# Kernel tuning notes

Measured on AMD Instinct MI355X. Metric: run time of the kernel, lower is better.

The kernel has to match this reference:

```python
import jax, jax.numpy as jnp
import numpy as np

C = 1024
D = C // 8      # query/key channels
R = C // 16     # channel-attention reduction
B, H, W = 4, 64, 64


def setup_inputs() -> dict:
    key = jax.random.key(0)
    ks = jax.random.split(key, 10)
    s = lambda k, shp, fan: jax.random.normal(k, shp, jnp.float32) * (1.0 / np.sqrt(fan))
    return {
        "x": jax.random.normal(ks[0], (B, C, H, W), jnp.float32),
        "x1": jax.random.normal(ks[1], (B, C, H, W), jnp.float32),
        "Wq": s(ks[2], (D, C), C), "bq": jnp.zeros((D,), jnp.float32),
        "Wk": s(ks[3], (D, C), C), "bk": jnp.zeros((D,), jnp.float32),
        "Wv": s(ks[4], (C, C), C), "bv": jnp.zeros((C,), jnp.float32),
        "Wca1": s(ks[5], (R, C), C),  # CBAM MLP, no bias
        "Wca2": s(ks[6], (C, R), R),
    }


def _forward(x, x1, Wq, bq, Wk, bk, Wv, bv, Wca1, Wca2):
    b, c, h, w = x.shape
    n = h * w
    # 1x1 convs as channel matmuls
    Q = (jnp.einsum('bchw,dc->bdhw', x, Wq) + bq[:, None, None]).reshape(b, D, n)   # [B,D,N]
    K = (jnp.einsum('bchw,dc->bdhw', x, Wk) + bk[:, None, None]).reshape(b, D, n)   # [B,D,N]
    V = (jnp.einsum('bchw,oc->bohw', x1, Wv) + bv[:, None, None]).reshape(b, c, n)  # [B,C,N]
    # energy[b,n,m] = Q[:,n] . K[:,m]
    energy = jnp.einsum('bdn,bdm->bnm', Q, K)
    att = jax.nn.sigmoid(energy)                       # [B,N,N]
    # torch: bmm(V, att^T) -> out[b,c,n] = sum_m V[b,c,m] * att[b,n,m]
    out = jnp.einsum('bcm,bnm->bcn', V, att).reshape(b, c, h, w)
    # ChannelAttention (CBAM): shared MLP on avg+max pooled features, sigmoid gate
    avg = out.mean(axis=(2, 3))                        # [B,C]
    mx = out.max(axis=(2, 3))                          # [B,C]
    mlp = lambda v: jnp.einsum('cr,br->bc', Wca2, jax.nn.relu(jnp.einsum('rc,bc->br', Wca1, v)))
    gate = jax.nn.sigmoid(mlp(avg) + mlp(mx))          # [B,C]
    return out * gate[:, :, None, None]


def reference(x, x1, Wq, bq, Wk, bk, Wv, bv, Wca1, Wca2):
    return _forward(x, x1, Wq, bq, Wk, bk, Wv, bv, Wca1, Wca2)
```

## Files before the change

### kernel.cpp

```cpp
#include <hip/hip_runtime.h>
#include <hip/hip_fp16.h>
#include <cstdint>

typedef _Float16 f16;
typedef __attribute__((ext_vector_type(8))) _Float16 half8;
typedef __attribute__((ext_vector_type(4))) float floatx4;

#define CC 1024
#define DD 128
#define RRR 64
#define BBATCH 4
#define NNN 4096

#define BM 128
#define BN 128

__device__ __forceinline__ void gl_lds16(const void* g, void* l) {
  __builtin_amdgcn_global_load_lds(
      (__attribute__((address_space(1))) void*)(uintptr_t)g,
      (__attribute__((address_space(3))) void*)l, 16, 0, 0);
}

template<int EPI, int BKT>
__global__ __launch_bounds__(256)
void gemm_bt(const f16* __restrict__ A, const f16* __restrict__ Bp, void* __restrict__ Cout,
             const float* __restrict__ bias, int M, int N, int K,
             int lda, int ldb, int ldc, size_t sA, size_t sB, size_t sC)
{
  constexpr int GPR = BKT / 8;
  constexpr int LOG2GPR = (BKT == 64) ? 3 : 4;
  constexpr int GIT = (BM * GPR) / 256;
  __shared__ __align__(16) f16 S[2 * BM * BKT];
  f16* As = S;
  f16* Bs = S + BM * BKT;

  const int z = blockIdx.z;
  const int tid  = threadIdx.x;
  const int lane = tid & 63;
  const int wave = tid >> 6;
  const int m0 = blockIdx.y * BM;
  const int n0 = blockIdx.x * BN;
  const int wm = (wave >> 1) * 64;
  const int wn = (wave & 1) * 64;
  const int quad = lane >> 4;
  const int r16  = lane & 15;
  const int rs   = r16 & 7;

  const f16* Ab = A  + (size_t)z * sA + (size_t)m0 * lda;
  const f16* Bb = Bp + (size_t)z * sB + (size_t)n0 * ldb;

  floatx4 acc[4][4];
#pragma unroll
  for (int i = 0; i < 4; ++i)
#pragma unroll
    for (int j = 0; j < 4; ++j)
      acc[i][j] = (floatx4){0.f, 0.f, 0.f, 0.f};

  int srow[GIT], ssrc[GIT];
#pragma unroll
  for (int r = 0; r < GIT; ++r) {
    const int gi = r * 256 + tid;
    const int row = gi >> LOG2GPR;
    const int gc  = gi & (GPR - 1);
    srow[r] = row;
    ssrc[r] = ((gc ^ (row & 7)) << 3);
  }

  for (int k0 = 0; k0 < K; k0 += BKT) {
#pragma unroll
    for (int r = 0; r < GIT; ++r) {
      gl_lds16(Ab + (size_t)srow[r] * lda + k0 + ssrc[r], As + (size_t)(r * 256 + tid) * 8);
      gl_lds16(Bb + (size_t)srow[r] * ldb + k0 + ssrc[r], Bs + (size_t)(r * 256 + tid) * 8);
    }
    __syncthreads();

#pragma unroll
    for (int kk = 0; kk < BKT; kk += 32) {
      const int kg = kk >> 3;
      half8 af[4], bfr[4];
#pragma unroll
      for (int i = 0; i < 4; ++i)
        af[i] = *(const half8*)(As + (wm + i * 16 + r16) * BKT + (((quad + kg) ^ rs) << 3));
#pragma unroll
      for (int j = 0; j < 4; ++j)
        bfr[j] = *(const half8*)(Bs + (wn + j * 16 + r16) * BKT + (((quad + kg) ^ rs) << 3));
#pragma unroll
      for (int i = 0; i < 4; ++i)
#pragma unroll
        for (int j = 0; j < 4; ++j)
          acc[i][j] = __builtin_amdgcn_mfma_f32_16x16x32_f16(af[i], bfr[j], acc[i][j], 0, 0, 0);
    }
    __syncthreads();
  }

  if constexpr (EPI == 0) {
    float* Cf = (float*)Cout + (size_t)z * sC;
#pragma unroll
    for (int i = 0; i < 4; ++i)
#pragma unroll
      for (int r = 0; r < 4; ++r) {
        const int row = m0 + wm + i * 16 + quad * 4 + r;
#pragma unroll
        for (int j = 0; j < 4; ++j)
          Cf[(size_t)row * ldc + n0 + wn + j * 16 + r16] = acc[i][j][r];
      }
  } else {
    f16* Ch = (f16*)Cout + (size_t)z * sC;
    f16* Ct = S;
#pragma unroll
    for (int i = 0; i < 4; ++i)
#pragma unroll
      for (int r = 0; r < 4; ++r) {
        const int rl = wm + i * 16 + quad * 4 + r;
#pragma unroll
        for (int j = 0; j < 4; ++j) {
          const int cl = wn + j * 16 + r16;
          const float v = acc[i][j][r];
          f16 h;
          if constexpr (EPI == 1)      h = (f16)(v + bias[m0 + rl]);
          else if constexpr (EPI == 2) h = (f16)(v + bias[n0 + cl]);
          else                         h = (f16)(1.0f / (1.0f + __expf(-v)));
          Ct[rl * BN + ((((cl >> 3) ^ (rl & 7)) << 3) | (cl & 7))] = h;
        }
      }
    __syncthreads();
#pragma unroll
    for (int p = 0; p < 8; ++p) {
      const int idx = p * 256 + tid;
      const int rl = idx >> 4;
      const int g  = idx & 15;
      half8 vv = *(const half8*)(Ct + rl * BN + (((g ^ (rl & 7))) << 3));
      *(half8*)(Ch + (size_t)(m0 + rl) * ldc + n0 + g * 8) = vv;
    }
  }
}

__global__ __launch_bounds__(256)
void prep(const float* __restrict__ Wq, const float* __restrict__ Wk, const float* __restrict__ Wv,
          const float* __restrict__ bq, const float* __restrict__ bk,
          f16* __restrict__ WQKb, f16* __restrict__ Wvb, float* __restrict__ bqk)
{
  const int NV = CC * CC;
  const int NQ = DD * CC;
  int i = blockIdx.x * 256 + threadIdx.x;
  if (i < NV)                    Wvb[i] = (f16)Wv[i];
  else if (i < NV + NQ)          WQKb[i - NV] = (f16)Wq[i - NV];
  else if (i < NV + 2 * NQ)      WQKb[i - NV] = (f16)Wk[i - NV - NQ];
  else if (i < NV + 2 * NQ + 2 * DD) {
    int t = i - NV - 2 * NQ;
    bqk[t] = (t < DD) ? bq[t] : bk[t - DD];
  }
}

__global__ __launch_bounds__(256)
void transpose_cvt(const float* __restrict__ x, const float* __restrict__ x1,
                   f16* __restrict__ ox, f16* __restrict__ ox1, int nb)
{
  const int zz = blockIdx.z;
  const int b  = (zz < nb) ? zz : zz - nb;
  const float* in = ((zz < nb) ? x : x1) + (size_t)b * CC * NNN;
  f16* out = ((zz < nb) ? ox : ox1) + (size_t)b * CC * NNN;
  __shared__ float tile[32][33];
  const int c0 = blockIdx.y * 32;
  const int n0 = blockIdx.x * 32;
  const int tx = threadIdx.x & 31;
  const int ty = threadIdx.x >> 5;
#pragma unroll
  for (int r = 0; r < 32; r += 8)
    tile[ty + r][tx] = in[(size_t)(c0 + ty + r) * NNN + n0 + tx];
  __syncthreads();
#pragma unroll
  for (int r = 0; r < 32; r += 8)
    out[(size_t)(n0 + ty + r) * CC + c0 + tx] = (f16)tile[tx][ty + r];
}

__global__ __launch_bounds__(256)
void rowreduce(const float* __restrict__ X, float* __restrict__ avg, float* __restrict__ mx, int ncols)
{
  const size_t ridx = (size_t)blockIdx.y * gridDim.x + blockIdx.x;
  const float4* p = (const float4*)(X + ridx * ncols);
  float s = 0.f, m = -3.402823466e38f;
  for (int i = threadIdx.x; i < ncols / 4; i += 256) {
    float4 v = p[i];
    s += v.x + v.y + v.z + v.w;
    m = fmaxf(m, fmaxf(fmaxf(v.x, v.y), fmaxf(v.z, v.w)));
  }
#pragma unroll
  for (int o = 32; o > 0; o >>= 1) {
    s += __shfl_down(s, o);
    m = fmaxf(m, __shfl_down(m, o));
  }
  __shared__ float ss[4], sm[4];
  if ((threadIdx.x & 63) == 0) { ss[threadIdx.x >> 6] = s; sm[threadIdx.x >> 6] = m; }
  __syncthreads();
  if (threadIdx.x == 0) {
    s = ss[0] + ss[1] + ss[2] + ss[3];
    m = fmaxf(fmaxf(sm[0], sm[1]), fmaxf(sm[2], sm[3]));
    avg[ridx] = s / (float)ncols;
    mx[ridx] = m;
  }
}

__global__ __launch_bounds__(256)
void mlp_gate(const float* __restrict__ avg, const float* __restrict__ mxv,
              const float* __restrict__ W1, const float* __restrict__ W2,
              float* __restrict__ gate)
{
  const int z = blockIdx.x;
  avg += (size_t)z * CC; mxv += (size_t)z * CC; gate += (size_t)z * CC;
  const int t = threadIdx.x;
  const int r = t & 63;
  const int part = t >> 6;
  __shared__ float pa[4][64], pm[4][64], h[RRR];
  {
    const float* w = W1 + (size_t)r * CC + part * 256;
    const float* av = avg + part * 256;
    const float* mv = mxv + part * 256;
    float sa = 0.f, sm = 0.f;
    for (int c = 0; c < 256; ++c) { float wv = w[c]; sa += wv * av[c]; sm += wv * mv[c]; }
    pa[part][r] = sa; pm[part][r] = sm;
  }
  __syncthreads();
  if (t < RRR) {
    float A_ = pa[0][t] + pa[1][t] + pa[2][t] + pa[3][t];
    float M_ = pm[0][t] + pm[1][t] + pm[2][t] + pm[3][t];
    h[t] = fmaxf(A_, 0.f) + fmaxf(M_, 0.f);
  }
  __syncthreads();
  for (int c = t; c < CC; c += 256) {
    float s = 0.f;
    for (int rr = 0; rr < RRR; ++rr) s += W2[(size_t)c * RRR + rr] * h[rr];
    gate[c] = 1.0f / (1.0f + __expf(-s));
  }
}

__global__ __launch_bounds__(256)
void scale_out(float* __restrict__ out, const float* __restrict__ gate)
{
  out  += (size_t)blockIdx.y * CC * NNN;
  gate += (size_t)blockIdx.y * CC;
  size_t i = (size_t)blockIdx.x * 256 + threadIdx.x;
  float4* p = (float4*)out;
  const float g = gate[(i * 4) >> 12];
  float4 v = p[i];
  v.x *= g; v.y *= g; v.z *= g; v.w *= g;
  p[i] = v;
}

extern "C" void kernel_launch(void* const* d_in, const int* in_sizes, int n_in,
                              void* d_out, int out_size, void* d_ws, size_t ws_size,
                              hipStream_t stream)
{
  const float* x    = (const float*)d_in[0];
  const float* x1   = (const float*)d_in[1];
  const float* Wq   = (const float*)d_in[2];
  const float* bq   = (const float*)d_in[3];
  const float* Wk   = (const float*)d_in[4];
  const float* bk   = (const float*)d_in[5];
  const float* Wv   = (const float*)d_in[6];
  const float* bv   = (const float*)d_in[7];
  const float* Wca1 = (const float*)d_in[8];
  const float* Wca2 = (const float*)d_in[9];
  float* out = (float*)d_out;

  char* ws = (char*)d_ws;
  size_t off = 0;
  auto alloc = [&](size_t bytes) { void* p = ws + off; off += (bytes + 255) & ~255ULL; return p; };

  f16* WQKb = (f16*)alloc((size_t)2 * DD * CC * 2);
  f16* Wvb  = (f16*)alloc((size_t)CC * CC * 2);
  float* bqk  = (float*)alloc(256 * 4);
  float* avg  = (float*)alloc((size_t)BBATCH * CC * 4);
  float* mxv  = (float*)alloc((size_t)BBATCH * CC * 4);
  float* gate = (float*)alloc((size_t)BBATCH * CC * 4);

  const size_t attB = (size_t)NNN * NNN * 2;
  const size_t xTB  = (size_t)BBATCH * NNN * CC * 2;
  const size_t qkB  = (size_t)BBATCH * NNN * 2 * DD * 2;
  const size_t vBB  = (size_t)BBATCH * CC * NNN * 2;
  const size_t fixedEnd = off;

  int g = 0;
  for (int cand = BBATCH; cand >= 1; cand >>= 1) {
    size_t need = fixedEnd + 2 * xTB + qkB + vBB + (size_t)cand * attB + (1 << 20);
    if (need <= ws_size) { g = cand; break; }
  }

  const dim3 blk(256);
  const int prepN = CC * CC + 2 * DD * CC + 2 * DD;
  prep<<<(prepN + 255) / 256, blk, 0, stream>>>(Wq, Wk, Wv, bq, bk, WQKb, Wvb, bqk);

  if (g > 0) {
    f16* xTb  = (f16*)alloc(xTB);
    f16* x1Tb = (f16*)alloc(xTB);
    f16* QKt  = (f16*)alloc(qkB);
    f16* Vb   = (f16*)alloc(vBB);
    f16* att  = (f16*)alloc((size_t)g * attB);

    transpose_cvt<<<dim3(NNN / 32, CC / 32, 2 * BBATCH), blk, 0, stream>>>(x, x1, xTb, x1Tb, BBATCH);

    gemm_bt<2, 64><<<dim3(2 * DD / BN, NNN / BM, BBATCH), blk, 0, stream>>>(
        xTb, WQKb, QKt, bqk, NNN, 2 * DD, CC,
        CC, CC, 2 * DD, (size_t)NNN * CC, 0, (size_t)NNN * 2 * DD);
    gemm_bt<1, 64><<<dim3(NNN / BN, CC / BM, BBATCH), blk, 0, stream>>>(
        Wvb, x1Tb, Vb, bv, CC, NNN, CC,
        CC, CC, NNN, 0, (size_t)NNN * CC, (size_t)CC * NNN);

    for (int b0 = 0; b0 < BBATCH; b0 += g) {
      const int gc = (b0 + g <= BBATCH) ? g : (BBATCH - b0);
      const size_t sQK = (size_t)NNN * 2 * DD;
      gemm_bt<3, 128><<<dim3(NNN / BN, NNN / BM, gc), blk, 0, stream>>>(
          QKt + (size_t)b0 * sQK, QKt + (size_t)b0 * sQK + DD, att, nullptr,
          NNN, NNN, DD, 2 * DD, 2 * DD, NNN, sQK, sQK, (size_t)NNN * NNN);
      gemm_bt<0, 64><<<dim3(NNN / BN, CC / BM, gc), blk, 0, stream>>>(
          Vb + (size_t)b0 * CC * NNN, att, out + (size_t)b0 * CC * NNN, nullptr,
          CC, NNN, NNN, NNN, NNN, NNN,
          (size_t)CC * NNN, (size_t)NNN * NNN, (size_t)CC * NNN);
    }

    rowreduce<<<dim3(CC, BBATCH), blk, 0, stream>>>(out, avg, mxv, NNN);
    mlp_gate<<<BBATCH, blk, 0, stream>>>(avg, mxv, Wca1, Wca2, gate);
    scale_out<<<dim3(CC * NNN / 4 / 256, BBATCH), blk, 0, stream>>>(out, gate);
  } else {
    f16* xTb  = (f16*)alloc((size_t)NNN * CC * 2);
    f16* x1Tb = (f16*)alloc((size_t)NNN * CC * 2);
    f16* QKt  = (f16*)alloc((size_t)NNN * 2 * DD * 2);
    f16* Vb   = (f16*)alloc((size_t)CC * NNN * 2);
    f16* att  = (f16*)alloc(attB);

    for (int b = 0; b < BBATCH; ++b) {
      const float* xb  = x  + (size_t)b * CC * NNN;
      const float* x1b = x1 + (size_t)b * CC * NNN;
      float* outb = out + (size_t)b * CC * NNN;

      transpose_cvt<<<dim3(NNN / 32, CC / 32, 2), blk, 0, stream>>>(xb, x1b, xTb, x1Tb, 1);

      gemm_bt<2, 64><<<dim3(2 * DD / BN, NNN / BM, 1), blk, 0, stream>>>(
          xTb, WQKb, QKt, bqk, NNN, 2 * DD, CC, CC, CC, 2 * DD, 0, 0, 0);
      gemm_bt<1, 64><<<dim3(NNN / BN, CC / BM, 1), blk, 0, stream>>>(
          Wvb, x1Tb, Vb, bv, CC, NNN, CC, CC, CC, NNN, 0, 0, 0);
      gemm_bt<3, 128><<<dim3(NNN / BN, NNN / BM, 1), blk, 0, stream>>>(
          QKt, QKt + DD, att, nullptr, NNN, NNN, DD, 2 * DD, 2 * DD, NNN, 0, 0, 0);
      gemm_bt<0, 64><<<dim3(NNN / BN, CC / BM, 1), blk, 0, stream>>>(
          Vb, att, outb, nullptr, CC, NNN, NNN, NNN, NNN, NNN, 0, 0, 0);

      rowreduce<<<dim3(CC, 1), blk, 0, stream>>>(outb, avg + (size_t)b * CC, mxv + (size_t)b * CC, NNN);
      mlp_gate<<<1, blk, 0, stream>>>(avg + (size_t)b * CC, mxv + (size_t)b * CC, Wca1, Wca2, gate + (size_t)b * CC);
      scale_out<<<dim3(CC * NNN / 4 / 256, 1), blk, 0, stream>>>(outb, gate + (size_t)b * CC);
    }
  }
}
```

Measured before the change: 543.6 us.

## Switch GEMMs to 32x32x16 MFMA and store attention output in fp16

Replaces the 16x16x32 MFMA tiling with 32x32x16 MFMA (2x2 per wave), so each wave issues fewer, larger matrix instructions and does fewer LDS fragment loads. The QK GEMM now uses BK=64 instead of 128. The V·att GEMM writes an fp16 intermediate through the LDS-staged coalesced epilogue instead of scattered fp32 stores. The row-reduce and scale kernels then read fp16 and write the final fp32 output, which cuts intermediate traffic but rounds the pre-gate output to fp16 and needs extra workspace.

```diff
diff --git a/kernel.cpp b/kernel.cpp
--- a/kernel.cpp
+++ b/kernel.cpp
@@ -4,7 +4,7 @@
 
 typedef _Float16 f16;
 typedef __attribute__((ext_vector_type(8))) _Float16 half8;
-typedef __attribute__((ext_vector_type(4))) float floatx4;
+typedef __attribute__((ext_vector_type(16))) float floatx16;
 
 #define CC 1024
 #define DD 128
@@ -14,6 +14,7 @@
 
 #define BM 128
 #define BN 128
+#define BK 64
 
 __device__ __forceinline__ void gl_lds16(const void* g, void* l) {
   __builtin_amdgcn_global_load_lds(
@@ -21,18 +22,15 @@
       (__attribute__((address_space(3))) void*)l, 16, 0, 0);
 }
 
-template<int EPI, int BKT>
-__global__ __launch_bounds__(256)
-void gemm_bt(const f16* __restrict__ A, const f16* __restrict__ Bp, void* __restrict__ Cout,
-             const float* __restrict__ bias, int M, int N, int K,
+template<int EPI>
+__global__ __launch_bounds__(256)
+void gemm_bt(const f16* __restrict__ A, const f16* __restrict__ Bp, f16* __restrict__ Cout,
+             const float* __restrict__ bias, int N, int K,
              int lda, int ldb, int ldc, size_t sA, size_t sB, size_t sC)
 {
-  constexpr int GPR = BKT / 8;
-  constexpr int LOG2GPR = (BKT == 64) ? 3 : 4;
-  constexpr int GIT = (BM * GPR) / 256;
-  __shared__ __align__(16) f16 S[2 * BM * BKT];
+  __shared__ __align__(16) f16 S[2 * BM * BK];
   f16* As = S;
-  f16* Bs = S + BM * BKT;
+  f16* Bs = S + BM * BK;
 
   const int z = blockIdx.z;
   const int tid  = threadIdx.x;
@@ -42,96 +40,85 @@
   const int n0 = blockIdx.x * BN;
   const int wm = (wave >> 1) * 64;
   const int wn = (wave & 1) * 64;
-  const int quad = lane >> 4;
-  const int r16  = lane & 15;
-  const int rs   = r16 & 7;
+  const int l31 = lane & 31;
+  const int hi  = lane >> 5;
+  const int rs  = lane & 7;
 
   const f16* Ab = A  + (size_t)z * sA + (size_t)m0 * lda;
   const f16* Bb = Bp + (size_t)z * sB + (size_t)n0 * ldb;
 
-  floatx4 acc[4][4];
-#pragma unroll
-  for (int i = 0; i < 4; ++i)
-#pragma unroll
-    for (int j = 0; j < 4; ++j)
-      acc[i][j] = (floatx4){0.f, 0.f, 0.f, 0.f};
-
-  int srow[GIT], ssrc[GIT];
-#pragma unroll
-  for (int r = 0; r < GIT; ++r) {
+  floatx16 acc[2][2];
+#pragma unroll
+  for (int i = 0; i < 2; ++i)
+#pragma unroll
+    for (int j = 0; j < 2; ++j)
+#pragma unroll
+      for (int r = 0; r < 16; ++r)
+        acc[i][j][r] = 0.f;
+
+  int srow[4], ssrc[4];
+#pragma unroll
+  for (int r = 0; r < 4; ++r) {
     const int gi = r * 256 + tid;
-    const int row = gi >> LOG2GPR;
-    const int gc  = gi & (GPR - 1);
+    const int row = gi >> 3;
+    const int gc  = gi & 7;
     srow[r] = row;
     ssrc[r] = ((gc ^ (row & 7)) << 3);
   }
 
-  for (int k0 = 0; k0 < K; k0 += BKT) {
-#pragma unroll
-    for (int r = 0; r < GIT; ++r) {
+  for (int k0 = 0; k0 < K; k0 += BK) {
+#pragma unroll
+    for (int r = 0; r < 4; ++r) {
       gl_lds16(Ab + (size_t)srow[r] * lda + k0 + ssrc[r], As + (size_t)(r * 256 + tid) * 8);
       gl_lds16(Bb + (size_t)srow[r] * ldb + k0 + ssrc[r], Bs + (size_t)(r * 256 + tid) * 8);
     }
     __syncthreads();
 
 #pragma unroll
-    for (int kk = 0; kk < BKT; kk += 32) {
-      const int kg = kk >> 3;
-      half8 af[4], bfr[4];
-#pragma unroll
-      for (int i = 0; i < 4; ++i)
-        af[i] = *(const half8*)(As + (wm + i * 16 + r16) * BKT + (((quad + kg) ^ rs) << 3));
-#pragma unroll
-      for (int j = 0; j < 4; ++j)
-        bfr[j] = *(const half8*)(Bs + (wn + j * 16 + r16) * BKT + (((quad + kg) ^ rs) << 3));
-#pragma unroll
-      for (int i = 0; i < 4; ++i)
-#pragma unroll
-        for (int j = 0; j < 4; ++j)
-          acc[i][j] = __builtin_amdgcn_mfma_f32_16x16x32_f16(af[i], bfr[j], acc[i][j], 0, 0, 0);
+    for (int kk = 0; kk < BK; kk += 16) {
+      const int gr = (((kk >> 3) + hi) ^ rs) << 3;
+      half8 af[2], bfr[2];
+#pragma unroll
+      for (int i = 0; i < 2; ++i)
+        af[i] = *(const half8*)(As + (wm + i * 32 + l31) * BK + gr);
+#pragma unroll
+      for (int j = 0; j < 2; ++j)
+        bfr[j] = *(const half8*)(Bs + (wn + j * 32 + l31) * BK + gr);
+#pragma unroll
+      for (int i = 0; i < 2; ++i)
+#pragma unroll
+        for (int j = 0; j < 2; ++j)
+          acc[i][j] = __builtin_amdgcn_mfma_f32_32x32x16_f16(af[i], bfr[j], acc[i][j], 0, 0, 0);
     }
     __syncthreads();
   }
 
-  if constexpr (EPI == 0) {
-    float* Cf = (float*)Cout + (size_t)z * sC;
-#pragma unroll
-    for (int i = 0; i < 4; ++i)
-#pragma unroll
-      for (int r = 0; r < 4; ++r) {
-        const int row = m0 + wm + i * 16 + quad * 4 + r;
-#pragma unroll
-        for (int j = 0; j < 4; ++j)
-          Cf[(size_t)row * ldc + n0 + wn + j * 16 + r16] = acc[i][j][r];
+  f16* Ch = Cout + (size_t)z * sC;
+  f16* Ct = S;
+#pragma unroll
+  for (int i = 0; i < 2; ++i)
+#pragma unroll
+    for (int j = 0; j < 2; ++j)
+#pragma unroll
+      for (int r = 0; r < 16; ++r) {
+        const int rl = wm + i * 32 + (r & 3) + 8 * (r >> 2) + 4 * hi;
+        const int cl = wn + j * 32 + l31;
+        const float v = acc[i][j][r];
+        f16 h;
+        if constexpr (EPI == 0)      h = (f16)v;
+        else if constexpr (EPI == 1) h = (f16)(v + bias[m0 + rl]);
+        else if constexpr (EPI == 2) h = (f16)(v + bias[n0 + cl]);
+        else                         h = (f16)(1.0f / (1.0f + __expf(-v)));
+        Ct[rl * BN + ((((cl >> 3) ^ (rl & 7)) << 3) | (cl & 7))] = h;
       }
-  } else {
-    f16* Ch = (f16*)Cout + (size_t)z * sC;
-    f16* Ct = S;
-#pragma unroll
-    for (int i = 0; i < 4; ++i)
-#pragma unroll
-      for (int r = 0; r < 4; ++r) {
-        const int rl = wm + i * 16 + quad * 4 + r;
-#pragma unroll
-        for (int j = 0; j < 4; ++j) {
-          const int cl = wn + j * 16 + r16;
-          const float v = acc[i][j][r];
-          f16 h;
-          if constexpr (EPI == 1)      h = (f16)(v + bias[m0 + rl]);
-          else if constexpr (EPI == 2) h = (f16)(v + bias[n0 + cl]);
-          else                         h = (f16)(1.0f / (1.0f + __expf(-v)));
-          Ct[rl * BN + ((((cl >> 3) ^ (rl & 7)) << 3) | (cl & 7))] = h;
-        }
-      }
-    __syncthreads();
-#pragma unroll
-    for (int p = 0; p < 8; ++p) {
-      const int idx = p * 256 + tid;
-      const int rl = idx >> 4;
-      const int g  = idx & 15;
-      half8 vv = *(const half8*)(Ct + rl * BN + (((g ^ (rl & 7))) << 3));
-      *(half8*)(Ch + (size_t)(m0 + rl) * ldc + n0 + g * 8) = vv;
-    }
+  __syncthreads();
+#pragma unroll
+  for (int p = 0; p < 8; ++p) {
+    const int idx = p * 256 + tid;
+    const int rl = idx >> 4;
+    const int g  = idx & 15;
+    half8 vv = *(const half8*)(Ct + rl * BN + ((g ^ (rl & 7)) << 3));
+    *(half8*)(Ch + (size_t)(m0 + rl) * ldc + n0 + g * 8) = vv;
   }
 }
 
@@ -175,15 +162,19 @@
 }
 
 __global__ __launch_bounds__(256)
-void rowreduce(const float* __restrict__ X, float* __restrict__ avg, float* __restrict__ mx, int ncols)
+void rowreduce(const f16* __restrict__ X, float* __restrict__ avg, float* __restrict__ mx, int ncols)
 {
   const size_t ridx = (size_t)blockIdx.y * gridDim.x + blockIdx.x;
-  const float4* p = (const float4*)(X + ridx * ncols);
+  const half8* p = (const half8*)(X + ridx * ncols);
   float s = 0.f, m = -3.402823466e38f;
-  for (int i = threadIdx.x; i < ncols / 4; i += 256) {
-    float4 v = p[i];
-    s += v.x + v.y + v.z + v.w;
-    m = fmaxf(m, fmaxf(fmaxf(v.x, v.y), fmaxf(v.z, v.w)));
+  for (int i = threadIdx.x; i < ncols / 8; i += 256) {
+    half8 v = p[i];
+#pragma unroll
+    for (int e = 0; e < 8; ++e) {
+      float f = (float)v[e];
+      s += f;
+      m = fmaxf(m, f);
+    }
   }
 #pragma unroll
   for (int o = 32; o > 0; o >>= 1) {
@@ -235,16 +226,19 @@
 }
 
 __global__ __launch_bounds__(256)
-void scale_out(float* __restrict__ out, const float* __restrict__ gate)
-{
-  out  += (size_t)blockIdx.y * CC * NNN;
+void scale_out(const f16* __restrict__ oh, float* __restrict__ out, const float* __restrict__ gate)
+{
+  oh  += (size_t)blockIdx.y * CC * NNN;
+  out += (size_t)blockIdx.y * CC * NNN;
   gate += (size_t)blockIdx.y * CC;
   size_t i = (size_t)blockIdx.x * 256 + threadIdx.x;
-  float4* p = (float4*)out;
-  const float g = gate[(i * 4) >> 12];
-  float4 v = p[i];
-  v.x *= g; v.y *= g; v.z *= g; v.w *= g;
-  p[i] = v;
+  half8 v = ((const half8*)oh)[i];
+  const float g = gate[(i * 8) >> 12];
+  float4 a = { (float)v[0] * g, (float)v[1] * g, (float)v[2] * g, (float)v[3] * g };
+  float4 b = { (float)v[4] * g, (float)v[5] * g, (float)v[6] * g, (float)v[7] * g };
+  float4* o = (float4*)out;
+  o[2 * i]     = a;
+  o[2 * i + 1] = b;
 }
 
 extern "C" void kernel_launch(void* const* d_in, const int* in_sizes, int n_in,
@@ -278,11 +272,12 @@
   const size_t xTB  = (size_t)BBATCH * NNN * CC * 2;
   const size_t qkB  = (size_t)BBATCH * NNN * 2 * DD * 2;
   const size_t vBB  = (size_t)BBATCH * CC * NNN * 2;
+  const size_t ohB  = (size_t)BBATCH * CC * NNN * 2;
   const size_t fixedEnd = off;
 
   int g = 0;
   for (int cand = BBATCH; cand >= 1; cand >>= 1) {
-    size_t need = fixedEnd + 2 * xTB + qkB + vBB + (size_t)cand * attB + (1 << 20);
+    size_t need = fixedEnd + 2 * xTB + qkB + vBB + ohB + (size_t)cand * attB + (1 << 20);
     if (need <= ws_size) { g = cand; break; }
   }
 
@@ -295,37 +290,39 @@
     f16* x1Tb = (f16*)alloc(xTB);
     f16* QKt  = (f16*)alloc(qkB);
     f16* Vb   = (f16*)alloc(vBB);
+    f16* outh = (f16*)alloc(ohB);
     f16* att  = (f16*)alloc((size_t)g * attB);
 
     transpose_cvt<<<dim3(NNN / 32, CC / 32, 2 * BBATCH), blk, 0, stream>>>(x, x1, xTb, x1Tb, BBATCH);
 
-    gemm_bt<2, 64><<<dim3(2 * DD / BN, NNN / BM, BBATCH), blk, 0, stream>>>(
-        xTb, WQKb, QKt, bqk, NNN, 2 * DD, CC,
+    gemm_bt<2><<<dim3(2 * DD / BN, NNN / BM, BBATCH), blk, 0, stream>>>(
+        xTb, WQKb, QKt, bqk, 2 * DD, CC,
         CC, CC, 2 * DD, (size_t)NNN * CC, 0, (size_t)NNN * 2 * DD);
-    gemm_bt<1, 64><<<dim3(NNN / BN, CC / BM, BBATCH), blk, 0, stream>>>(
-        Wvb, x1Tb, Vb, bv, CC, NNN, CC,
+    gemm_bt<1><<<dim3(NNN / BN, CC / BM, BBATCH), blk, 0, stream>>>(
+        Wvb, x1Tb, Vb, bv, NNN, CC,
         CC, CC, NNN, 0, (size_t)NNN * CC, (size_t)CC * NNN);
 
     for (int b0 = 0; b0 < BBATCH; b0 += g) {
       const int gc = (b0 + g <= BBATCH) ? g : (BBATCH - b0);
       const size_t sQK = (size_t)NNN * 2 * DD;
-      gemm_bt<3, 128><<<dim3(NNN / BN, NNN / BM, gc), blk, 0, stream>>>(
+      gemm_bt<3><<<dim3(NNN / BN, NNN / BM, gc), blk, 0, stream>>>(
           QKt + (size_t)b0 * sQK, QKt + (size_t)b0 * sQK + DD, att, nullptr,
-          NNN, NNN, DD, 2 * DD, 2 * DD, NNN, sQK, sQK, (size_t)NNN * NNN);
-      gemm_bt<0, 64><<<dim3(NNN / BN, CC / BM, gc), blk, 0, stream>>>(
-          Vb + (size_t)b0 * CC * NNN, att, out + (size_t)b0 * CC * NNN, nullptr,
-          CC, NNN, NNN, NNN, NNN, NNN,
+          NNN, DD, 2 * DD, 2 * DD, NNN, sQK, sQK, (size_t)NNN * NNN);
+      gemm_bt<0><<<dim3(NNN / BN, CC / BM, gc), blk, 0, stream>>>(
+          Vb + (size_t)b0 * CC * NNN, att, outh + (size_t)b0 * CC * NNN, nullptr,
+          NNN, NNN, NNN, NNN, NNN,
           (size_t)CC * NNN, (size_t)NNN * NNN, (size_t)CC * NNN);
     }
 
-    rowreduce<<<dim3(CC, BBATCH), blk, 0, stream>>>(out, avg, mxv, NNN);
+    rowreduce<<<dim3(CC, BBATCH), blk, 0, stream>>>(outh, avg, mxv, NNN);
     mlp_gate<<<BBATCH, blk, 0, stream>>>(avg, mxv, Wca1, Wca2, gate);
-    scale_out<<<dim3(CC * NNN / 4 / 256, BBATCH), blk, 0, stream>>>(out, gate);
+    scale_out<<<dim3(CC * NNN / 8 / 256, BBATCH), blk, 0, stream>>>(outh, out, gate);
   } else {
     f16* xTb  = (f16*)alloc((size_t)NNN * CC * 2);
     f16* x1Tb = (f16*)alloc((size_t)NNN * CC * 2);
     f16* QKt  = (f16*)alloc((size_t)NNN * 2 * DD * 2);
     f16* Vb   = (f16*)alloc((size_t)CC * NNN * 2);
+    f16* outh = (f16*)alloc((size_t)CC * NNN * 2);
     f16* att  = (f16*)alloc(attB);
 
     for (int b = 0; b < BBATCH; ++b) {
@@ -335,18 +332,18 @@
 
       transpose_cvt<<<dim3(NNN / 32, CC / 32, 2), blk, 0, stream>>>(xb, x1b, xTb, x1Tb, 1);
 
-      gemm_bt<2, 64><<<dim3(2 * DD / BN, NNN / BM, 1), blk, 0, stream>>>(
-          xTb, WQKb, QKt, bqk, NNN, 2 * DD, CC, CC, CC, 2 * DD, 0, 0, 0);
-      gemm_bt<1, 64><<<dim3(NNN / BN, CC / BM, 1), blk, 0, stream>>>(
-          Wvb, x1Tb, Vb, bv, CC, NNN, CC, CC, CC, NNN, 0, 0, 0);
-      gemm_bt<3, 128><<<dim3(NNN / BN, NNN / BM, 1), blk, 0, stream>>>(
-          QKt, QKt + DD, att, nullptr, NNN, NNN, DD, 2 * DD, 2 * DD, NNN, 0, 0, 0);
-      gemm_bt<0, 64><<<dim3(NNN / BN, CC / BM, 1), blk, 0, stream>>>(
-          Vb, att, outb, nullptr, CC, NNN, NNN, NNN, NNN, NNN, 0, 0, 0);
-
-      rowreduce<<<dim3(CC, 1), blk, 0, stream>>>(outb, avg + (size_t)b * CC, mxv + (size_t)b * CC, NNN);
+      gemm_bt<2><<<dim3(2 * DD / BN, NNN / BM, 1), blk, 0, stream>>>(
+          xTb, WQKb, QKt, bqk, 2 * DD, CC, CC, CC, 2 * DD, 0, 0, 0);
+      gemm_bt<1><<<dim3(NNN / BN, CC / BM, 1), blk, 0, stream>>>(
+          Wvb, x1Tb, Vb, bv, NNN, CC, CC, CC, NNN, 0, 0, 0);
+      gemm_bt<3><<<dim3(NNN / BN, NNN / BM, 1), blk, 0, stream>>>(
+          QKt, QKt + DD, att, nullptr, NNN, DD, 2 * DD, 2 * DD, NNN, 0, 0, 0);
+      gemm_bt<0><<<dim3(NNN / BN, CC / BM, 1), blk, 0, stream>>>(
+          Vb, att, outh, nullptr, NNN, NNN, NNN, NNN, NNN, 0, 0, 0);
+
+      rowreduce<<<dim3(CC, 1), blk, 0, stream>>>(outh, avg + (size_t)b * CC, mxv + (size_t)b * CC, NNN);
       mlp_gate<<<1, blk, 0, stream>>>(avg + (size_t)b * CC, mxv + (size_t)b * CC, Wca1, Wca2, gate + (size_t)b * CC);
-      scale_out<<<dim3(CC * NNN / 4 / 256, 1), blk, 0, stream>>>(outb, gate + (size_t)b * CC);
-    }
-  }
-}
+      scale_out<<<dim3(CC * NNN / 8 / 256, 1), blk, 0, stream>>>(outh, outb, gate + (size_t)b * CC);
+    }
+  }
+}
```

After: 517.1 us. 1.05x faster.
